# Kernel tuning notes

Measured on AMD Instinct MI355X. Metric: run time of the kernel, lower is better.

The kernel has to match this reference:

```python
import jax, jax.numpy as jnp
import numpy as np

B, T, C, N = 4, 2048, 1024, 16
D = C // N


def setup_inputs() -> dict:
    key = jax.random.key(0)
    ks = jax.random.split(key, 10)
    s = 1.0 / np.sqrt(C)
    x = jax.random.normal(ks[0], (B, T, C), dtype=jnp.float32)
    token_mask = jax.random.randint(ks[1], (B, T), 0, 2, dtype=jnp.int32)
    token_mask = token_mask.at[:, 0].set(1)  # keep col 0 valid so no all--inf row
    inp = {"x": x, "token_mask": token_mask}
    for i, name in enumerate(["q", "k", "v", "p"]):
        inp[f"w{name}"] = jax.random.uniform(ks[2 + 2 * i], (C, C), jnp.float32, -s, s)
        inp[f"b{name}"] = jax.random.uniform(ks[3 + 2 * i], (C,), jnp.float32, -s, s)
    return inp


def reference(x, token_mask, wq, bq, wk, bk, wv, bv, wp, bp):
    # projections: nn.Linear computes x @ W.T + b
    q = (x @ wq.T + bq).reshape(B, T, N, D)
    k = (x @ wk.T + bk).reshape(B, T, N, D)
    v = (x @ wv.T + bv).reshape(B, T, N, D)
    # scores: (B, N, T, T)
    scores = jnp.einsum("bqnd,bknd->bnqk", q, k) / jnp.sqrt(jnp.float32(D))
    causal = jnp.tril(jnp.ones((T, T), dtype=bool))
    valid = causal[None, None] & (token_mask[:, None, None, :] != 0)
    scores = jnp.where(valid, scores, -jnp.inf)
    probs = jax.nn.softmax(scores, axis=-1)
    attn = jnp.einsum("bnqk,bknd->bqnd", probs, v).reshape(B, T, C)
    out = attn @ wp.T + bp
    return out
```

## Files before the change

kernel.cpp:

```cpp
#include <hip/hip_runtime.h>
#include <hip/hip_bf16.h>
#include <math.h>

typedef short bf16x8 __attribute__((ext_vector_type(8)));
typedef float f32x4 __attribute__((ext_vector_type(4)));

#if __has_builtin(__builtin_amdgcn_exp2f)
#define EXP2F(x) __builtin_amdgcn_exp2f(x)
#else
#define EXP2F(x) __expf(0.69314718056f * (x))
#endif

__device__ __forceinline__ unsigned short f2bf(float f) {
    union { float f; unsigned u; } v; v.f = f;
    unsigned r = v.u + 0x7fffu + ((v.u >> 16) & 1u);
    return (unsigned short)(r >> 16);
}

__device__ __forceinline__ unsigned pack_bf2(float a, float b) {
    __hip_bfloat162 h = __float22bfloat162_rn(float2{a, b});
    union { __hip_bfloat162 h; unsigned u; } c; c.h = h;
    return c.u;
}

__device__ __forceinline__ void gld_lds16(const unsigned short* g, const unsigned short* l) {
    __builtin_amdgcn_global_load_lds(
        (const __attribute__((address_space(1))) void*)g,
        (__attribute__((address_space(3))) void*)l, 16, 0, 0);
}

__global__ void cvt_f32_bf16(const float* __restrict__ src, unsigned short* __restrict__ dst, int n) {
    int i = (blockIdx.x * blockDim.x + threadIdx.x) * 4;
    if (i < n) {
        float4 f = *(const float4*)(src + i);
        ushort4 o;
        o.x = f2bf(f.x); o.y = f2bf(f.y); o.z = f2bf(f.z); o.w = f2bf(f.w);
        *(ushort4*)(dst + i) = o;
    }
}

__global__ void cvt4_f32_bf16(const float* s0, const float* s1, const float* s2, const float* s3,
                              unsigned short* d0, unsigned short* d1, unsigned short* d2,
                              unsigned short* d3, int n) {
    const float* s; unsigned short* d;
    switch (blockIdx.y) {
        case 0: s = s0; d = d0; break;
        case 1: s = s1; d = d1; break;
        case 2: s = s2; d = d2; break;
        default: s = s3; d = d3; break;
    }
    int i = (blockIdx.x * blockDim.x + threadIdx.x) * 4;
    if (i < n) {
        float4 f = *(const float4*)(s + i);
        ushort4 o;
        o.x = f2bf(f.x); o.y = f2bf(f.y); o.z = f2bf(f.z); o.w = f2bf(f.w);
        *(ushort4*)(d + i) = o;
    }
}

__global__ __launch_bounds__(256) void gemm_bt(
        const unsigned short* __restrict__ A, const unsigned short* __restrict__ W,
        const float* __restrict__ b0p, const float* __restrict__ b1p,
        const float* __restrict__ b2p, float* __restrict__ outF,
        unsigned short* __restrict__ outB, int M, int Nlog, int K) {
    __shared__ __align__(16) unsigned short As[128][32];
    __shared__ __align__(16) unsigned short Ws[128][32];
    const size_t BUFS = (size_t)8192 * 1024;
    const int m0 = blockIdx.y * 128, n0 = blockIdx.x * 128;
    const int tid = threadIdx.x, lane = tid & 63, w = tid >> 6;
    const int quad = lane >> 4, lc = lane & 15;
    const int wr = (w >> 1) * 64, wc = (w & 1) * 64;
    const int sr = lane >> 2, sc = (lane & 3) * 8;

    const int buf = n0 >> 10;
    const float* bias = buf == 0 ? b0p : (buf == 1 ? b1p : b2p);

    f32x4 acc[4][4] = {};

    for (int k0 = 0; k0 < K; k0 += 32) {
        __syncthreads();
        gld_lds16(A + (size_t)(m0 + w * 32 +      sr) * K + k0 + sc, &As[w * 32     ][0]);
        gld_lds16(A + (size_t)(m0 + w * 32 + 16 + sr) * K + k0 + sc, &As[w * 32 + 16][0]);
        gld_lds16(W + (size_t)(n0 + w * 32 +      sr) * K + k0 + sc, &Ws[w * 32     ][0]);
        gld_lds16(W + (size_t)(n0 + w * 32 + 16 + sr) * K + k0 + sc, &Ws[w * 32 + 16][0]);
        __syncthreads();
        bf16x8 af[4], bw[4];
        #pragma unroll
        for (int i = 0; i < 4; ++i) af[i] = *(const bf16x8*)&As[wr + i * 16 + lc][quad * 8];
        #pragma unroll
        for (int j = 0; j < 4; ++j) bw[j] = *(const bf16x8*)&Ws[wc + j * 16 + lc][quad * 8];
        #pragma unroll
        for (int i = 0; i < 4; ++i)
            #pragma unroll
            for (int j = 0; j < 4; ++j)
                acc[i][j] = __builtin_amdgcn_mfma_f32_16x16x32_bf16(af[i], bw[j], acc[i][j], 0, 0, 0);
    }

    #pragma unroll
    for (int j = 0; j < 4; ++j) {
        int col = n0 + wc + j * 16 + lc;
        int coll = col & 1023;
        float bj = bias[coll];
        #pragma unroll
        for (int i = 0; i < 4; ++i) {
            int rowb = m0 + wr + i * 16 + quad * 4;
            #pragma unroll
            for (int r = 0; r < 4; ++r) {
                float v = acc[i][j][r] + bj;
                size_t idx = (size_t)buf * BUFS + (size_t)(rowb + r) * 1024 + coll;
                if (outB) outB[idx] = f2bf(v);
                else      outF[idx] = v;
            }
        }
    }
}

__global__ __launch_bounds__(256, 4) void attn_kernel(
        const unsigned short* __restrict__ Q, const unsigned short* __restrict__ K,
        const unsigned short* __restrict__ V, const int* __restrict__ tmask,
        unsigned short* __restrict__ O) {
    const int T = 2048, C = 1024;
    __shared__ __align__(16) unsigned short Kl[64][72];
    __shared__ __align__(16) unsigned short VT[64][72];
    __shared__ __align__(16) unsigned short Pl[4][16][72];
    __shared__ float maskf[64];

    const int pair = blockIdx.x;
    const int bn = blockIdx.y;
    const int b = bn >> 4, h = bn & 15;
    const int tid = threadIdx.x, w = tid >> 6, lane = tid & 63;
    const int quad = lane >> 4, lc = lane & 15;
    const float NEG_INF = -__builtin_inff();
    const float CSC = 0.18033688011112042f;

    #pragma unroll 1
    for (int half = 0; half < 2; ++half) {
        const int qt = half ? (31 - pair) : pair;

        size_t qrow = (size_t)(b * T + qt * 64 + w * 16 + lc) * C + h * 64;
        bf16x8 qb0 = *(const bf16x8*)(Q + qrow + quad * 8);
        bf16x8 qb1 = *(const bf16x8*)(Q + qrow + 32 + quad * 8);

        f32x4 oaccT[4] = {};
        float m = NEG_INF, l = 0.f;
        const int qg = qt * 64 + w * 16 + lc;

        auto step = [&](int kt, bool DIAG) {
            __syncthreads();
            {
                int r = tid >> 2, c16 = (tid & 3) * 16;
                size_t g = (size_t)(b * T + kt * 64 + r) * C + h * 64 + c16;
                *(bf16x8*)&Kl[r][c16]     = *(const bf16x8*)(K + g);
                *(bf16x8*)&Kl[r][c16 + 8] = *(const bf16x8*)(K + g + 8);
            }
            {
                int r0 = (tid & 31) * 2, c8 = (tid >> 5) * 8;
                size_t g = (size_t)(b * T + kt * 64 + r0) * C + h * 64 + c8;
                bf16x8 v0 = *(const bf16x8*)(V + g);
                bf16x8 v1 = *(const bf16x8*)(V + g + C);
                #pragma unroll
                for (int i = 0; i < 8; ++i) {
                    unsigned pk = (unsigned short)v0[i] | ((unsigned)(unsigned short)v1[i] << 16);
                    *(unsigned*)&VT[c8 + i][r0] = pk;
                }
            }
            if (tid < 64)
                maskf[tid] = tmask[b * T + kt * 64 + tid] ? 0.0f : NEG_INF;
            __syncthreads();

            f32x4 sacc[4] = {};
            #pragma unroll
            for (int j = 0; j < 4; ++j) {
                bf16x8 ka0 = *(const bf16x8*)&Kl[j * 16 + lc][quad * 8];
                bf16x8 ka1 = *(const bf16x8*)&Kl[j * 16 + lc][32 + quad * 8];
                sacc[j] = __builtin_amdgcn_mfma_f32_16x16x32_bf16(ka0, qb0, sacc[j], 0, 0, 0);
                sacc[j] = __builtin_amdgcn_mfma_f32_16x16x32_bf16(ka1, qb1, sacc[j], 0, 0, 0);
            }

            float s[4][4];
            float mx = NEG_INF;
            #pragma unroll
            for (int j = 0; j < 4; ++j) {
                f32x4 mk = *(const f32x4*)&maskf[j * 16 + quad * 4];
                #pragma unroll
                for (int r = 0; r < 4; ++r) {
                    float sv = fmaf(sacc[j][r], CSC, mk[r]);
                    if (DIAG) {
                        int kg = kt * 64 + j * 16 + quad * 4 + r;
                        if (kg > qg) sv = NEG_INF;
                    }
                    s[j][r] = sv;
                    mx = fmaxf(mx, sv);
                }
            }
            mx = fmaxf(mx, __shfl_xor(mx, 16, 64));
            mx = fmaxf(mx, __shfl_xor(mx, 32, 64));
            float mnew = fmaxf(m, mx);
            float alpha = EXP2F(m - mnew);
            m = mnew;
            float ps = 0.f;
            #pragma unroll
            for (int j = 0; j < 4; ++j)
                #pragma unroll
                for (int r = 0; r < 4; ++r) {
                    float p = EXP2F(s[j][r] - mnew);
                    s[j][r] = p;
                    ps += p;
                }
            ps += __shfl_xor(ps, 16, 64);
            ps += __shfl_xor(ps, 32, 64);
            l = l * alpha + ps;
            #pragma unroll
            for (int jd = 0; jd < 4; ++jd) oaccT[jd] *= alpha;

            #pragma unroll
            for (int j = 0; j < 4; ++j) {
                uint2 pk;
                pk.x = pack_bf2(s[j][0], s[j][1]);
                pk.y = pack_bf2(s[j][2], s[j][3]);
                *(uint2*)&Pl[w][lc][j * 16 + quad * 4] = pk;
            }
            bf16x8 pb0 = *(const bf16x8*)&Pl[w][lc][quad * 8];
            bf16x8 pb1 = *(const bf16x8*)&Pl[w][lc][32 + quad * 8];

            #pragma unroll
            for (int jd = 0; jd < 4; ++jd) {
                bf16x8 va0 = *(const bf16x8*)&VT[jd * 16 + lc][quad * 8];
                bf16x8 va1 = *(const bf16x8*)&VT[jd * 16 + lc][32 + quad * 8];
                oaccT[jd] = __builtin_amdgcn_mfma_f32_16x16x32_bf16(va0, pb0, oaccT[jd], 0, 0, 0);
                oaccT[jd] = __builtin_amdgcn_mfma_f32_16x16x32_bf16(va1, pb1, oaccT[jd], 0, 0, 0);
            }
        };

        #pragma unroll 1
        for (int kt = 0; kt < qt; ++kt) step(kt, false);
        step(qt, true);

        float inv = 1.0f / l;
        size_t orow = (size_t)(b * T + qt * 64 + w * 16 + lc) * C + h * 64;
        #pragma unroll
        for (int jd = 0; jd < 4; ++jd) {
            ushort4 o4;
            o4.x = f2bf(oaccT[jd][0] * inv);
            o4.y = f2bf(oaccT[jd][1] * inv);
            o4.z = f2bf(oaccT[jd][2] * inv);
            o4.w = f2bf(oaccT[jd][3] * inv);
            *(ushort4*)(O + orow + jd * 16 + quad * 4) = o4;
        }
    }
}

extern "C" void kernel_launch(void* const* d_in, const int* in_sizes, int n_in,
                              void* d_out, int out_size, void* d_ws, size_t ws_size,
                              hipStream_t stream) {
    const float* x  = (const float*)d_in[0];
    const int* tm   = (const int*)d_in[1];
    const float* wq = (const float*)d_in[2]; const float* bq = (const float*)d_in[3];
    const float* wk = (const float*)d_in[4]; const float* bk = (const float*)d_in[5];
    const float* wv = (const float*)d_in[6]; const float* bv = (const float*)d_in[7];
    const float* wp = (const float*)d_in[8]; const float* bp = (const float*)d_in[9];
    float* out = (float*)d_out;

    const int Bv = 4, Tv = 2048, Cv = 1024;
    const size_t MT = (size_t)Bv * Tv;
    const size_t XN = MT * Cv;
    const size_t WN = (size_t)Cv * Cv;

    unsigned short* xb  = (unsigned short*)d_ws;
    unsigned short* wqb = xb  + XN;
    unsigned short* wkb = wqb + WN;
    unsigned short* wvb = wkb + WN;
    unsigned short* wpb = wvb + WN;
    unsigned short* Qb  = wpb + WN;
    unsigned short* Kb  = Qb + XN;
    unsigned short* Vb  = Kb + XN;
    unsigned short* Ab  = xb;

    cvt_f32_bf16<<<XN / 1024, 256, 0, stream>>>(x, xb, (int)XN);
    cvt4_f32_bf16<<<dim3(WN / 1024, 4), 256, 0, stream>>>(wq, wk, wv, wp, wqb, wkb, wvb, wpb, (int)WN);

    gemm_bt<<<dim3(24, 64), 256, 0, stream>>>(xb, wqb, bq, bk, bv, nullptr, Qb, (int)MT, 3072, Cv);

    attn_kernel<<<dim3(16, Bv * 16), 256, 0, stream>>>(Qb, Kb, Vb, tm, Ab);

    gemm_bt<<<dim3(8, 64), 256, 0, stream>>>(Ab, wpb, bp, bp, bp, out, nullptr, (int)MT, 1024, Cv);
}
```

Measured before the change: 310.7 us.

## Prefetch K/V tiles into swizzled LDS, write V transposed from QKV GEMM

The QKV GEMM epilogue now writes V directly in a per-head transposed layout, so the attention kernel no longer transposes V through LDS with scalar stores. K and V tiles are loaded with direct global-to-LDS copies into XOR-swizzled unpadded buffers, and V is double-buffered so the next tile's loads are issued during the current tile's softmax and PV MFMAs. The token mask is precomputed once as additive floats in a scratch area of the output buffer and read from global memory. This adds a small kernel launch and a scattered V store pattern in the GEMM, and it relies on the output buffer being overwritten later by the final GEMM.

```diff
diff --git a/kernel.cpp b/kernel.cpp
--- a/kernel.cpp
+++ b/kernel.cpp
@@ -58,11 +58,17 @@
     }
 }
 
+__global__ void mask_to_f(const int* __restrict__ tm, float* __restrict__ ma, int n) {
+    int i = blockIdx.x * blockDim.x + threadIdx.x;
+    if (i < n) ma[i] = tm[i] ? 0.0f : -__builtin_inff();
+}
+
 __global__ __launch_bounds__(256) void gemm_bt(
         const unsigned short* __restrict__ A, const unsigned short* __restrict__ W,
         const float* __restrict__ b0p, const float* __restrict__ b1p,
         const float* __restrict__ b2p, float* __restrict__ outF,
-        unsigned short* __restrict__ outB, int M, int Nlog, int K) {
+        unsigned short* __restrict__ outB, unsigned short* __restrict__ vt,
+        int M, int Nlog, int K) {
     __shared__ __align__(16) unsigned short As[128][32];
     __shared__ __align__(16) unsigned short Ws[128][32];
     const size_t BUFS = (size_t)8192 * 1024;
@@ -104,12 +110,23 @@
         #pragma unroll
         for (int i = 0; i < 4; ++i) {
             int rowb = m0 + wr + i * 16 + quad * 4;
-            #pragma unroll
-            for (int r = 0; r < 4; ++r) {
-                float v = acc[i][j][r] + bj;
-                size_t idx = (size_t)buf * BUFS + (size_t)(rowb + r) * 1024 + coll;
-                if (outB) outB[idx] = f2bf(v);
-                else      outF[idx] = v;
+            if (buf == 2) {
+                int bb = rowb >> 11, t = rowb & 2047;
+                int hh = coll >> 6, dd = coll & 63;
+                ushort4 o4;
+                o4.x = f2bf(acc[i][j][0] + bj);
+                o4.y = f2bf(acc[i][j][1] + bj);
+                o4.z = f2bf(acc[i][j][2] + bj);
+                o4.w = f2bf(acc[i][j][3] + bj);
+                *(ushort4*)(vt + ((size_t)(bb * 16 + hh) * 64 + dd) * 2048 + t) = o4;
+            } else {
+                #pragma unroll
+                for (int r = 0; r < 4; ++r) {
+                    float v = acc[i][j][r] + bj;
+                    size_t idx = (size_t)buf * BUFS + (size_t)(rowb + r) * 1024 + coll;
+                    if (outB) outB[idx] = f2bf(v);
+                    else      outF[idx] = v;
+                }
             }
         }
     }
@@ -117,13 +134,12 @@
 
 __global__ __launch_bounds__(256, 4) void attn_kernel(
         const unsigned short* __restrict__ Q, const unsigned short* __restrict__ K,
-        const unsigned short* __restrict__ V, const int* __restrict__ tmask,
+        const unsigned short* __restrict__ Vt, const float* __restrict__ maskadd,
         unsigned short* __restrict__ O) {
     const int T = 2048, C = 1024;
-    __shared__ __align__(16) unsigned short Kl[64][72];
-    __shared__ __align__(16) unsigned short VT[64][72];
+    __shared__ __align__(16) unsigned short Kl[64][64];
+    __shared__ __align__(16) unsigned short Vl[2][64][64];
     __shared__ __align__(16) unsigned short Pl[4][16][72];
-    __shared__ float maskf[64];
 
     const int pair = blockIdx.x;
     const int bn = blockIdx.y;
@@ -133,10 +149,34 @@
     const float NEG_INF = -__builtin_inff();
     const float CSC = 0.18033688011112042f;
 
+    const unsigned short* Kbh = K + (size_t)b * T * C + h * 64;
+    const unsigned short* Vbh = Vt + (size_t)(b * 16 + h) * 64 * 2048;
+
+    const int lrow = lane >> 3;
+    const int swz8 = ((lane & 7) ^ (lrow & 7)) * 8;
+    const int kb0 = (quad ^ (lc & 7)) * 8;
+
+    auto stageK = [&](int kt) {
+        #pragma unroll
+        for (int ch = 0; ch < 2; ++ch)
+            gld_lds16(Kbh + (size_t)(kt * 64 + w * 16 + ch * 8 + lrow) * C + swz8,
+                      &Kl[w * 16 + ch * 8][0]);
+    };
+    auto stageV = [&](int kt, int s) {
+        #pragma unroll
+        for (int ch = 0; ch < 2; ++ch)
+            gld_lds16(Vbh + (size_t)(w * 16 + ch * 8 + lrow) * 2048 + kt * 64 + swz8,
+                      &Vl[s][w * 16 + ch * 8][0]);
+    };
+
     #pragma unroll 1
     for (int half = 0; half < 2; ++half) {
         const int qt = half ? (31 - pair) : pair;
 
+        if (half) __syncthreads();
+        stageK(0);
+        stageV(0, 0);
+
         size_t qrow = (size_t)(b * T + qt * 64 + w * 16 + lc) * C + h * 64;
         bf16x8 qb0 = *(const bf16x8*)(Q + qrow + quad * 8);
         bf16x8 qb1 = *(const bf16x8*)(Q + qrow + 32 + quad * 8);
@@ -145,47 +185,39 @@
         float m = NEG_INF, l = 0.f;
         const int qg = qt * 64 + w * 16 + lc;
 
-        auto step = [&](int kt, bool DIAG) {
+        #pragma unroll 1
+        for (int kt = 0; kt <= qt; ++kt) {
+            const int slot = kt & 1;
             __syncthreads();
-            {
-                int r = tid >> 2, c16 = (tid & 3) * 16;
-                size_t g = (size_t)(b * T + kt * 64 + r) * C + h * 64 + c16;
-                *(bf16x8*)&Kl[r][c16]     = *(const bf16x8*)(K + g);
-                *(bf16x8*)&Kl[r][c16 + 8] = *(const bf16x8*)(K + g + 8);
-            }
-            {
-                int r0 = (tid & 31) * 2, c8 = (tid >> 5) * 8;
-                size_t g = (size_t)(b * T + kt * 64 + r0) * C + h * 64 + c8;
-                bf16x8 v0 = *(const bf16x8*)(V + g);
-                bf16x8 v1 = *(const bf16x8*)(V + g + C);
-                #pragma unroll
-                for (int i = 0; i < 8; ++i) {
-                    unsigned pk = (unsigned short)v0[i] | ((unsigned)(unsigned short)v1[i] << 16);
-                    *(unsigned*)&VT[c8 + i][r0] = pk;
-                }
-            }
-            if (tid < 64)
-                maskf[tid] = tmask[b * T + kt * 64 + tid] ? 0.0f : NEG_INF;
-            __syncthreads();
+
+            f32x4 mk[4];
+            #pragma unroll
+            for (int j = 0; j < 4; ++j)
+                mk[j] = *(const f32x4*)(maskadd + b * T + kt * 64 + j * 16 + quad * 4);
 
             f32x4 sacc[4] = {};
             #pragma unroll
             for (int j = 0; j < 4; ++j) {
-                bf16x8 ka0 = *(const bf16x8*)&Kl[j * 16 + lc][quad * 8];
-                bf16x8 ka1 = *(const bf16x8*)&Kl[j * 16 + lc][32 + quad * 8];
+                bf16x8 ka0 = *(const bf16x8*)&Kl[j * 16 + lc][kb0];
+                bf16x8 ka1 = *(const bf16x8*)&Kl[j * 16 + lc][kb0 ^ 32];
                 sacc[j] = __builtin_amdgcn_mfma_f32_16x16x32_bf16(ka0, qb0, sacc[j], 0, 0, 0);
                 sacc[j] = __builtin_amdgcn_mfma_f32_16x16x32_bf16(ka1, qb1, sacc[j], 0, 0, 0);
             }
 
+            __syncthreads();
+            if (kt < qt) {
+                stageK(kt + 1);
+                stageV(kt + 1, slot ^ 1);
+            }
+
             float s[4][4];
             float mx = NEG_INF;
             #pragma unroll
             for (int j = 0; j < 4; ++j) {
-                f32x4 mk = *(const f32x4*)&maskf[j * 16 + quad * 4];
                 #pragma unroll
                 for (int r = 0; r < 4; ++r) {
-                    float sv = fmaf(sacc[j][r], CSC, mk[r]);
-                    if (DIAG) {
+                    float sv = fmaf(sacc[j][r], CSC, mk[j][r]);
+                    if (kt == qt) {
                         int kg = kt * 64 + j * 16 + quad * 4 + r;
                         if (kg > qg) sv = NEG_INF;
                     }
@@ -225,16 +257,12 @@
 
             #pragma unroll
             for (int jd = 0; jd < 4; ++jd) {
-                bf16x8 va0 = *(const bf16x8*)&VT[jd * 16 + lc][quad * 8];
-                bf16x8 va1 = *(const bf16x8*)&VT[jd * 16 + lc][32 + quad * 8];
+                bf16x8 va0 = *(const bf16x8*)&Vl[slot][jd * 16 + lc][kb0];
+                bf16x8 va1 = *(const bf16x8*)&Vl[slot][jd * 16 + lc][kb0 ^ 32];
                 oaccT[jd] = __builtin_amdgcn_mfma_f32_16x16x32_bf16(va0, pb0, oaccT[jd], 0, 0, 0);
                 oaccT[jd] = __builtin_amdgcn_mfma_f32_16x16x32_bf16(va1, pb1, oaccT[jd], 0, 0, 0);
             }
-        };
-
-        #pragma unroll 1
-        for (int kt = 0; kt < qt; ++kt) step(kt, false);
-        step(qt, true);
+        }
 
         float inv = 1.0f / l;
         size_t orow = (size_t)(b * T + qt * 64 + w * 16 + lc) * C + h * 64;
@@ -273,15 +301,17 @@
     unsigned short* wpb = wvb + WN;
     unsigned short* Qb  = wpb + WN;
     unsigned short* Kb  = Qb + XN;
-    unsigned short* Vb  = Kb + XN;
+    unsigned short* Vtb = Kb + XN;
     unsigned short* Ab  = xb;
+    float* maskadd = (float*)d_out;
 
     cvt_f32_bf16<<<XN / 1024, 256, 0, stream>>>(x, xb, (int)XN);
     cvt4_f32_bf16<<<dim3(WN / 1024, 4), 256, 0, stream>>>(wq, wk, wv, wp, wqb, wkb, wvb, wpb, (int)WN);
-
-    gemm_bt<<<dim3(24, 64), 256, 0, stream>>>(xb, wqb, bq, bk, bv, nullptr, Qb, (int)MT, 3072, Cv);
-
-    attn_kernel<<<dim3(16, Bv * 16), 256, 0, stream>>>(Qb, Kb, Vb, tm, Ab);
-
-    gemm_bt<<<dim3(8, 64), 256, 0, stream>>>(Ab, wpb, bp, bp, bp, out, nullptr, (int)MT, 1024, Cv);
-}
+    mask_to_f<<<(int)(MT / 256), 256, 0, stream>>>(tm, maskadd, (int)MT);
+
+    gemm_bt<<<dim3(24, 64), 256, 0, stream>>>(xb, wqb, bq, bk, bv, nullptr, Qb, Vtb, (int)MT, 3072, Cv);
+
+    attn_kernel<<<dim3(16, Bv * 16), 256, 0, stream>>>(Qb, Kb, Vtb, maskadd, Ab);
+
+    gemm_bt<<<dim3(8, 64), 256, 0, stream>>>(Ab, wpb, bp, bp, bp, out, nullptr, nullptr, (int)MT, 1024, Cv);
+}
```

New measurement: 310.2 us. Within noise of the previous version (-0.2%).
